# Performance work log

Measured on AMD Instinct MI355X. Metric: run time of the kernel, lower is better.

The kernel has to match this reference:

```python
import jax, jax.numpy as jnp
import numpy as np

N = 20000        # nodes
E = 320000       # edges (before self-loops)
V = 5000         # vocab size for each of the 5 categorical fields
L = 20           # padded token list length per node
SF = 16          # scalar feature count
ED = 32          # embedding_dim
HC = 128         # hidden_channels
NH = 4           # num_heads (conv1)
B = 8            # graphs in batch
DIN = SF + 5 * ED  # 176


def setup_inputs() -> dict:
    key = jax.random.key(0)
    ks = jax.random.split(key, 24)
    inp = {
        "x_scalar": jax.random.normal(ks[0], (N, SF), jnp.float32),
        "x_opcode": jax.random.randint(ks[1], (N, L), 0, V),
        "x_source": jax.random.randint(ks[2], (N, L), 0, V),
        "x_sink": jax.random.randint(ks[3], (N, L), 0, V),
        "x_string_manip": jax.random.randint(ks[4], (N, L), 0, V),
        "x_payload": jax.random.randint(ks[5], (N, L), 0, V),
        "edge_index": jax.random.randint(ks[6], (2, E), 0, N),
        "batch": jnp.sort(jax.random.randint(ks[7], (N,), 0, B)),
        # embedding tables (padding row 0 contributes nothing via the mask)
        "emb_opcode": jax.random.normal(ks[8], (V, ED), jnp.float32),
        "emb_source": jax.random.normal(ks[9], (V, ED), jnp.float32),
        "emb_sink": jax.random.normal(ks[10], (V, ED), jnp.float32),
        "emb_string_manip": jax.random.normal(ks[11], (V, ED), jnp.float32),
        "emb_payload": jax.random.normal(ks[12], (V, ED), jnp.float32),
        # LayerNorm params
        "ln_g": jnp.ones((DIN,), jnp.float32),
        "ln_b": jnp.zeros((DIN,), jnp.float32),
        # GATConv 1: in=DIN, out=HC, heads=NH
        "W1": jax.random.normal(ks[13], (DIN, NH * HC), jnp.float32) / np.sqrt(DIN),
        "a_src1": jax.random.normal(ks[14], (NH, HC), jnp.float32) / np.sqrt(HC),
        "a_dst1": jax.random.normal(ks[15], (NH, HC), jnp.float32) / np.sqrt(HC),
        "b1": jnp.zeros((NH * HC,), jnp.float32),
        # GATConv 2: in=NH*HC, out=HC, heads=1
        "W2": jax.random.normal(ks[16], (NH * HC, HC), jnp.float32) / np.sqrt(NH * HC),
        "a_src2": jax.random.normal(ks[17], (1, HC), jnp.float32) / np.sqrt(HC),
        "a_dst2": jax.random.normal(ks[18], (1, HC), jnp.float32) / np.sqrt(HC),
        "b2": jnp.zeros((HC,), jnp.float32),
    }
    return inp


def _masked_mean(table, idx):
    # embeds * (idx != 0) summed over token dim, divided by token count
    emb = table[idx]                                   # [N, L, ED]
    mask = (idx != 0).astype(table.dtype)[..., None]   # [N, L, 1]
    return (emb * mask).sum(1) / (mask.sum(1) + 1e-9)


def _layer_norm(x, g, b, eps=1e-5):
    mu = x.mean(-1, keepdims=True)
    var = ((x - mu) ** 2).mean(-1, keepdims=True)
    return (x - mu) * jax.lax.rsqrt(var + eps) * g + b


def _gat(x, src, dst, W, a_src, a_dst, bias, n):
    # PyG GATConv (eval mode: attention dropout off), self-loops already in src/dst
    h_, c = a_src.shape
    h = (x @ W).reshape(n, h_, c)                      # [N, H, C]
    al_s = (h * a_src).sum(-1)                         # [N, H]
    al_d = (h * a_dst).sum(-1)                         # [N, H]
    e = jax.nn.leaky_relu(al_s[src] + al_d[dst], 0.2)  # [E, H]
    m = jax.ops.segment_max(e, dst, num_segments=n)    # per-dst max for stability
    ex = jnp.exp(e - m[dst])
    den = jax.ops.segment_sum(ex, dst, num_segments=n)
    alpha = ex / (den[dst] + 1e-16)                    # per-dst softmax
    msg = h[src] * alpha[:, :, None]                   # [E, H, C]
    out = jax.ops.segment_sum(msg, dst, num_segments=n)
    return out.reshape(n, h_ * c) + bias


def reference(x_scalar, x_opcode, x_source, x_sink, x_string_manip, x_payload,
              edge_index, batch,
              emb_opcode, emb_source, emb_sink, emb_string_manip, emb_payload,
              ln_g, ln_b, W1, a_src1, a_dst1, b1, W2, a_src2, a_dst2, b2):
    n = x_scalar.shape[0]
    feats = jnp.concatenate([
        x_scalar,
        _masked_mean(emb_opcode, x_opcode),
        _masked_mean(emb_source, x_source),
        _masked_mean(emb_sink, x_sink),
        _masked_mean(emb_string_manip, x_string_manip),
        _masked_mean(emb_payload, x_payload),
    ], axis=1)                                         # [N, DIN]
    # GATConv adds self-loops by default
    loops = jnp.arange(n, dtype=edge_index.dtype)
    src = jnp.concatenate([edge_index[0], loops])
    dst = jnp.concatenate([edge_index[1], loops])
    x = jax.nn.elu(_gat(_layer_norm(feats, ln_g, ln_b), src, dst, W1, a_src1, a_dst1, b1, n))
    x = jax.nn.elu(_gat(x, src, dst, W2, a_src2, a_dst2, b2, n))
    return jax.ops.segment_max(x, batch, num_segments=B)  # global_max_pool -> [B, HC]
```

## Files before the change

### kernel.cpp

```cpp
#include <hip/hip_runtime.h>
#include <math.h>

#define SF 16
#define ED 32
#define LTOK 20
#define DIN 176
#define KP1 192
#define HC 128

typedef _Float16 f16x8 __attribute__((ext_vector_type(8)));
typedef _Float16 f16x2 __attribute__((ext_vector_type(2)));
typedef float f32x4 __attribute__((ext_vector_type(4)));

#if defined(__has_builtin)
#if __has_builtin(__builtin_amdgcn_fdot2)
#define HAVE_FDOT2 1
#endif
#endif

static __device__ __forceinline__ float leaky02(float x) { return x >= 0.f ? x : 0.2f * x; }
static __device__ __forceinline__ float eluf(float x)    { return x > 0.f ? x : expm1f(x); }
static __device__ __forceinline__ unsigned short f2h(float f)
{
  _Float16 h = (_Float16)f;
  return __builtin_bit_cast(unsigned short, h);
}
static __device__ __forceinline__ float h2f(unsigned short u)
{
  return (float)__builtin_bit_cast(_Float16, u);
}
static __device__ __forceinline__ float readlane_f(float v, int j)
{
  return __int_as_float(__builtin_amdgcn_readlane(__float_as_int(v), j));
}
static __device__ __forceinline__ unsigned readlane_u(unsigned v, int j)
{
  return (unsigned)__builtin_amdgcn_readlane((int)v, j);
}
#ifdef HAVE_FDOT2
static __device__ __forceinline__ float dot2(unsigned w, unsigned f, float c)
{
  return __builtin_amdgcn_fdot2(__builtin_bit_cast(f16x2, w),
                                __builtin_bit_cast(f16x2, f), c, false);
}
#endif

__global__ __launch_bounds__(256)
void prep_combined_kernel(const float* __restrict__ W1, const float* __restrict__ W2,
                          unsigned short* __restrict__ W1t, unsigned short* __restrict__ W2t,
                          const float* __restrict__ as1, const float* __restrict__ ad1,
                          float* __restrict__ vs, float* __restrict__ vd,
                          int* __restrict__ deg, unsigned* __restrict__ pool,
                          float* __restrict__ als2, float* __restrict__ ald2,
                          int N, int poolN)
{
  const int nb1 = (512 * KP1 + 255) / 256;
  const int nb2 = (HC * 512 + 255) / 256;
  const int nb3 = (N + 255) / 256;
  const int nb4 = (poolN + 255) / 256;
  int bid = blockIdx.x;
  if (bid < nb1) {
    int i = bid * 256 + threadIdx.x;
    if (i < 512 * KP1) {
      int n = i / KP1, k = i - n * KP1;
      W1t[i] = f2h((k < DIN) ? W1[(size_t)k * 512 + n] : 0.f);
    }
    return;
  }
  bid -= nb1;
  if (bid < nb2) {
    int i = bid * 256 + threadIdx.x;
    if (i < HC * 512) {
      int n = i / 512, k = i - n * 512;
      W2t[i] = f2h(W2[(size_t)k * HC + n]);
    }
    return;
  }
  bid -= nb2;
  if (bid < nb3) {
    int i = bid * 256 + threadIdx.x;
    if (i < N) { deg[i] = 0; als2[i] = 0.f; ald2[i] = 0.f; }
    return;
  }
  bid -= nb3;
  if (bid < nb4) {
    int i = bid * 256 + threadIdx.x;
    if (i < poolN) pool[i] = 0x00800000u;
    return;
  }
  bid -= nb4;
  {
    int k = bid;
    int h = threadIdx.x >> 6, lane = threadIdx.x & 63;
    const float* row = W1 + (size_t)k * 512 + h * HC;
    float s = row[lane] * as1[h * HC + lane] + row[lane + 64] * as1[h * HC + lane + 64];
    float d = row[lane] * ad1[h * HC + lane] + row[lane + 64] * ad1[h * HC + lane + 64];
    #pragma unroll
    for (int off = 32; off; off >>= 1) { s += __shfl_down(s, off); d += __shfl_down(d, off); }
    if (lane == 0) { vs[k * 4 + h] = s; vd[k * 4 + h] = d; }
  }
}

__global__ __launch_bounds__(256)
void feat_ln_kernel(const float* __restrict__ xs,
                    const int* __restrict__ i0, const int* __restrict__ i1,
                    const int* __restrict__ i2, const int* __restrict__ i3,
                    const int* __restrict__ i4,
                    const float* __restrict__ e0, const float* __restrict__ e1,
                    const float* __restrict__ e2, const float* __restrict__ e3,
                    const float* __restrict__ e4,
                    const float* __restrict__ g, const float* __restrict__ b,
                    const float4* __restrict__ vs, const float4* __restrict__ vd,
                    unsigned short* __restrict__ out,
                    float* __restrict__ als, float* __restrict__ ald, int N)
{
  __shared__ int toks[4][5 * LTOK];
  int w = threadIdx.x >> 6, l = threadIdx.x & 63;
  int n = blockIdx.x * 4 + w;
  if (n >= N) return;

  for (int q = l; q < 5 * LTOK; q += 64) {
    int f = q / LTOK, j = q - f * LTOK;
    const int* ip = (f == 0) ? i0 : (f == 1) ? i1 : (f == 2) ? i2 : (f == 3) ? i3 : i4;
    toks[w][q] = ip[n * LTOK + j];
  }

  float v[3];
  #pragma unroll
  for (int r = 0; r < 3; ++r) {
    int c = l + r * 64;
    float val = 0.f;
    if (c < SF) {
      val = xs[n * SF + c];
    } else if (c < DIN) {
      int f  = (c - SF) >> 5;
      int ch = (c - SF) & 31;
      const float* ep = (f == 0) ? e0 : (f == 1) ? e1 : (f == 2) ? e2 : (f == 3) ? e3 : e4;
      float vals[LTOK];
      #pragma unroll
      for (int j = 0; j < LTOK; ++j)
        vals[j] = ep[toks[w][f * LTOK + j] * ED + ch];
      float sum = 0.f, cnt = 0.f;
      #pragma unroll
      for (int j = 0; j < LTOK; ++j)
        if (toks[w][f * LTOK + j] != 0) { sum += vals[j]; cnt += 1.f; }
      val = sum / (cnt + 1e-9f);
    }
    v[r] = val;
  }

  float p  = v[0] + v[1] + v[2];
  float p2 = v[0] * v[0] + v[1] * v[1] + v[2] * v[2];
  #pragma unroll
  for (int off = 32; off; off >>= 1) { p += __shfl_xor(p, off); p2 += __shfl_xor(p2, off); }
  float mu   = p * (1.f / DIN);
  float var  = fmaxf(p2 * (1.f / DIN) - mu * mu, 0.f);
  float rstd = rsqrtf(var + 1e-5f);

  float pr[8] = {0.f, 0.f, 0.f, 0.f, 0.f, 0.f, 0.f, 0.f};
  #pragma unroll
  for (int r = 0; r < 3; ++r) {
    int c = l + r * 64;
    float y = 0.f;
    if (c < DIN) {
      y = (v[r] - mu) * rstd * g[c] + b[c];
      float4 s4 = vs[c], d4 = vd[c];
      pr[0] += y * s4.x; pr[1] += y * s4.y; pr[2] += y * s4.z; pr[3] += y * s4.w;
      pr[4] += y * d4.x; pr[5] += y * d4.y; pr[6] += y * d4.z; pr[7] += y * d4.w;
    }
    if (c < KP1) out[(size_t)n * KP1 + c] = f2h(y);
  }
  #pragma unroll
  for (int j = 0; j < 8; ++j)
    #pragma unroll
    for (int off = 32; off; off >>= 1) pr[j] += __shfl_xor(pr[j], off);
  if (l == 0) {
    als[n * 4 + 0] = pr[0]; als[n * 4 + 1] = pr[1];
    als[n * 4 + 2] = pr[2]; als[n * 4 + 3] = pr[3];
    ald[n * 4 + 0] = pr[4]; ald[n * 4 + 1] = pr[5];
    ald[n * 4 + 2] = pr[6]; ald[n * 4 + 3] = pr[7];
  }
}

__global__ void count_kernel(const int* __restrict__ ei, int E, int N, int* __restrict__ deg)
{
  int e = blockIdx.x * blockDim.x + threadIdx.x;
  if (e < E + N) {
    int dst = (e < E) ? ei[E + e] : (e - E);
    atomicAdd(&deg[dst], 1);
  }
}

__global__ __launch_bounds__(1024)
void scan_kernel(const int* __restrict__ deg, int* __restrict__ rowptr,
                 int* __restrict__ fill, int N)
{
  __shared__ int sums[1024];
  int t = threadIdx.x;
  int CH = (N + 1023) >> 10;
  int base = t * CH;
  int s = 0;
  for (int i = 0; i < CH; ++i) if (base + i < N) s += deg[base + i];
  sums[t] = s;
  __syncthreads();
  for (int off = 1; off < 1024; off <<= 1) {
    int v = (t >= off) ? sums[t - off] : 0;
    __syncthreads();
    sums[t] += v;
    __syncthreads();
  }
  int run = sums[t] - s;
  for (int i = 0; i < CH; ++i) {
    if (base + i < N) {
      rowptr[base + i] = run;
      fill[base + i]   = run;
      run += deg[base + i];
    }
  }
  if (t == 1023) rowptr[N] = run;
}

__global__ void scatter_kernel(const int* __restrict__ ei, int E, int N,
                               int* __restrict__ fill, int* __restrict__ csr_src)
{
  int e = blockIdx.x * blockDim.x + threadIdx.x;
  if (e < E + N) {
    int src, dst;
    if (e < E) { src = ei[e]; dst = ei[E + e]; }
    else       { src = dst = e - E; }
    int pos = atomicAdd(&fill[dst], 1);
    csr_src[pos] = src;
  }
}

__global__ __launch_bounds__(256)
void agg_feat_kernel(const unsigned short* __restrict__ F,
                     const float4* __restrict__ als, const float4* __restrict__ ald,
                     const int* __restrict__ rowptr, const int* __restrict__ csr_src,
                     unsigned short* __restrict__ G, int N)
{
  int wv = threadIdx.x >> 6, lane = threadIdx.x & 63;
  int n = blockIdx.x * 4 + wv;
  if (n >= N) return;
  int rs = __builtin_amdgcn_readfirstlane(rowptr[n]);
  int re = __builtin_amdgcn_readfirstlane(rowptr[n + 1]);
  int cnt = re - rs;
  float4 ad4 = ald[n];
  float aldv[4] = { ad4.x, ad4.y, ad4.z, ad4.w };

  float acc[4][4] = {};
  bool act = lane < 48;
  const unsigned short* Fb = F + lane * 4;

#ifdef HAVE_FDOT2
  auto passB = [&](int srcA, unsigned pkw[4], int ccnt) {
    for (int j = 0; j < ccnt; j += 4) {
      int s0 = __builtin_amdgcn_readlane(srcA, j);
      int s1 = __builtin_amdgcn_readlane(srcA, j + 1);
      int s2 = __builtin_amdgcn_readlane(srcA, j + 2);
      int s3 = __builtin_amdgcn_readlane(srcA, j + 3);
      unsigned wa0 = readlane_u(pkw[0], j), wb0 = readlane_u(pkw[0], j + 2);
      unsigned wa1 = readlane_u(pkw[1], j), wb1 = readlane_u(pkw[1], j + 2);
      unsigned wa2 = readlane_u(pkw[2], j), wb2 = readlane_u(pkw[2], j + 2);
      unsigned wa3 = readlane_u(pkw[3], j), wb3 = readlane_u(pkw[3], j + 2);
      if (act) {
        int2 a0 = *(const int2*)(Fb + (size_t)s0 * KP1);
        int2 a1 = *(const int2*)(Fb + (size_t)s1 * KP1);
        int2 a2 = *(const int2*)(Fb + (size_t)s2 * KP1);
        int2 a3 = *(const int2*)(Fb + (size_t)s3 * KP1);
        unsigned pA = __builtin_amdgcn_perm((unsigned)a0.x, (unsigned)a1.x, 0x01000504u);
        unsigned pB = __builtin_amdgcn_perm((unsigned)a0.x, (unsigned)a1.x, 0x03020706u);
        unsigned pC = __builtin_amdgcn_perm((unsigned)a0.y, (unsigned)a1.y, 0x01000504u);
        unsigned pD = __builtin_amdgcn_perm((unsigned)a0.y, (unsigned)a1.y, 0x03020706u);
        unsigned qA = __builtin_amdgcn_perm((unsigned)a2.x, (unsigned)a3.x, 0x01000504u);
        unsigned qB = __builtin_amdgcn_perm((unsigned)a2.x, (unsigned)a3.x, 0x03020706u);
        unsigned qC = __builtin_amdgcn_perm((unsigned)a2.y, (unsigned)a3.y, 0x01000504u);
        unsigned qD = __builtin_amdgcn_perm((unsigned)a2.y, (unsigned)a3.y, 0x03020706u);
        acc[0][0] = dot2(wa0, pA, acc[0][0]); acc[0][1] = dot2(wa0, pB, acc[0][1]);
        acc[0][2] = dot2(wa0, pC, acc[0][2]); acc[0][3] = dot2(wa0, pD, acc[0][3]);
        acc[1][0] = dot2(wa1, pA, acc[1][0]); acc[1][1] = dot2(wa1, pB, acc[1][1]);
        acc[1][2] = dot2(wa1, pC, acc[1][2]); acc[1][3] = dot2(wa1, pD, acc[1][3]);
        acc[2][0] = dot2(wa2, pA, acc[2][0]); acc[2][1] = dot2(wa2, pB, acc[2][1]);
        acc[2][2] = dot2(wa2, pC, acc[2][2]); acc[2][3] = dot2(wa2, pD, acc[2][3]);
        acc[3][0] = dot2(wa3, pA, acc[3][0]); acc[3][1] = dot2(wa3, pB, acc[3][1]);
        acc[3][2] = dot2(wa3, pC, acc[3][2]); acc[3][3] = dot2(wa3, pD, acc[3][3]);
        acc[0][0] = dot2(wb0, qA, acc[0][0]); acc[0][1] = dot2(wb0, qB, acc[0][1]);
        acc[0][2] = dot2(wb0, qC, acc[0][2]); acc[0][3] = dot2(wb0, qD, acc[0][3]);
        acc[1][0] = dot2(wb1, qA, acc[1][0]); acc[1][1] = dot2(wb1, qB, acc[1][1]);
        acc[1][2] = dot2(wb1, qC, acc[1][2]); acc[1][3] = dot2(wb1, qD, acc[1][3]);
        acc[2][0] = dot2(wb2, qA, acc[2][0]); acc[2][1] = dot2(wb2, qB, acc[2][1]);
        acc[2][2] = dot2(wb2, qC, acc[2][2]); acc[2][3] = dot2(wb2, qD, acc[2][3]);
        acc[3][0] = dot2(wb3, qA, acc[3][0]); acc[3][1] = dot2(wb3, qB, acc[3][1]);
        acc[3][2] = dot2(wb3, qC, acc[3][2]); acc[3][3] = dot2(wb3, qD, acc[3][3]);
      }
    }
  };
#else
  auto passB = [&](int srcA, float wf[4], int ccnt) {
    for (int j = 0; j < ccnt; ++j) {
      int src = __builtin_amdgcn_readlane(srcA, j);
      float q0 = readlane_f(wf[0], j), q1 = readlane_f(wf[1], j);
      float q2 = readlane_f(wf[2], j), q3 = readlane_f(wf[3], j);
      if (act) {
        int2 a0 = *(const int2*)(Fb + (size_t)src * KP1);
        float f0 = h2f((unsigned short)(a0.x & 0xffff));
        float f1 = h2f((unsigned short)((unsigned)a0.x >> 16));
        float f2v = h2f((unsigned short)(a0.y & 0xffff));
        float f3 = h2f((unsigned short)((unsigned)a0.y >> 16));
        acc[0][0] += q0 * f0; acc[0][1] += q0 * f1; acc[0][2] += q0 * f2v; acc[0][3] += q0 * f3;
        acc[1][0] += q1 * f0; acc[1][1] += q1 * f1; acc[1][2] += q1 * f2v; acc[1][3] += q1 * f3;
        acc[2][0] += q2 * f0; acc[2][1] += q2 * f1; acc[2][2] += q2 * f2v; acc[2][3] += q2 * f3;
        acc[3][0] += q3 * f0; acc[3][1] += q3 * f1; acc[3][2] += q3 * f2v; acc[3][3] += q3 * f3;
      }
    }
  };
#endif

  if (cnt <= 64) {
    int srcA = 0;
    float e[4] = { -1e30f, -1e30f, -1e30f, -1e30f };
    if (lane < cnt) {
      srcA = csr_src[rs + lane];
      float4 a4 = als[srcA];
      e[0] = leaky02(a4.x + aldv[0]); e[1] = leaky02(a4.y + aldv[1]);
      e[2] = leaky02(a4.z + aldv[2]); e[3] = leaky02(a4.w + aldv[3]);
    }
    float m[4] = { e[0], e[1], e[2], e[3] };
    #pragma unroll
    for (int off = 32; off; off >>= 1)
      #pragma unroll
      for (int h = 0; h < 4; ++h) m[h] = fmaxf(m[h], __shfl_xor(m[h], off));
    float w[4];
    #pragma unroll
    for (int h = 0; h < 4; ++h) w[h] = (lane < cnt) ? __expf(e[h] - m[h]) : 0.f;
    float den[4] = { w[0], w[1], w[2], w[3] };
    #pragma unroll
    for (int off = 32; off; off >>= 1)
      #pragma unroll
      for (int h = 0; h < 4; ++h) den[h] += __shfl_xor(den[h], off);
    #pragma unroll
    for (int h = 0; h < 4; ++h) w[h] /= (den[h] + 1e-16f);
#ifdef HAVE_FDOT2
    unsigned pkw[4];
    #pragma unroll
    for (int h = 0; h < 4; ++h) {
      float wn = __shfl_xor(w[h], 1);
      float we = (lane & 1) ? wn : w[h];
      float wo = (lane & 1) ? w[h] : wn;
      pkw[h] = (unsigned)f2h(we) | ((unsigned)f2h(wo) << 16);
    }
    passB(srcA, pkw, cnt);
#else
    passB(srcA, w, cnt);
#endif
  } else {
    float m[4], s[4];
    #pragma unroll
    for (int h = 0; h < 4; ++h) { m[h] = -1e30f; s[h] = 0.f; }
    for (int i = rs + lane; i < re; i += 64) {
      int src = csr_src[i];
      float4 a4 = als[src];
      float av[4] = { a4.x, a4.y, a4.z, a4.w };
      #pragma unroll
      for (int h = 0; h < 4; ++h) {
        float e = leaky02(av[h] + aldv[h]);
        float Mx = fmaxf(m[h], e);
        s[h] = s[h] * __expf(m[h] - Mx) + __expf(e - Mx);
        m[h] = Mx;
      }
    }
    #pragma unroll
    for (int off = 32; off; off >>= 1) {
      #pragma unroll
      for (int h = 0; h < 4; ++h) {
        float m2 = __shfl_xor(m[h], off);
        float s2 = __shfl_xor(s[h], off);
        float Mx = fmaxf(m[h], m2);
        s[h] = s[h] * __expf(m[h] - Mx) + s2 * __expf(m2 - Mx);
        m[h] = Mx;
      }
    }
    float inv[4];
    #pragma unroll
    for (int h = 0; h < 4; ++h) inv[h] = 1.f / (s[h] + 1e-16f);
    for (int b0 = rs; b0 < re; b0 += 64) {
      int bcnt = min(64, re - b0);
      int srcA = 0;
      float w[4] = {0.f, 0.f, 0.f, 0.f};
      if (lane < bcnt) {
        srcA = csr_src[b0 + lane];
        float4 a4 = als[srcA];
        w[0] = __expf(leaky02(a4.x + aldv[0]) - m[0]) * inv[0];
        w[1] = __expf(leaky02(a4.y + aldv[1]) - m[1]) * inv[1];
        w[2] = __expf(leaky02(a4.z + aldv[2]) - m[2]) * inv[2];
        w[3] = __expf(leaky02(a4.w + aldv[3]) - m[3]) * inv[3];
      }
#ifdef HAVE_FDOT2
      unsigned pkw[4];
      #pragma unroll
      for (int h = 0; h < 4; ++h) {
        float wn = __shfl_xor(w[h], 1);
        float we = (lane & 1) ? wn : w[h];
        float wo = (lane & 1) ? w[h] : wn;
        pkw[h] = (unsigned)f2h(we) | ((unsigned)f2h(wo) << 16);
      }
      passB(srcA, pkw, bcnt);
#else
      passB(srcA, w, bcnt);
#endif
    }
  }

  if (act) {
    #pragma unroll
    for (int h = 0; h < 4; ++h) {
      int2 o;
      o.x = (int)f2h(acc[h][0]) | ((int)f2h(acc[h][1]) << 16);
      o.y = (int)f2h(acc[h][2]) | ((int)f2h(acc[h][3]) << 16);
      *(int2*)&G[((size_t)h * N + n) * KP1 + lane * 4] = o;
    }
  }
}

template<int KPad, int BIAS_ELU, int LOGITS>
__global__ __launch_bounds__(256)
void gemm64_kernel(const unsigned short* __restrict__ A,
                   const unsigned short* __restrict__ Bt,
                   unsigned short* __restrict__ C,
                   int M, int Nc,
                   size_t aStrideZ, size_t bStrideZ, int cColStrideZ,
                   const float* __restrict__ bias,
                   const float* __restrict__ la_s, const float* __restrict__ la_d,
                   float* __restrict__ lout_s, float* __restrict__ lout_d)
{
  A  += blockIdx.z * aStrideZ;
  Bt += blockIdx.z * bStrideZ;
  const int colZ = blockIdx.z * cColStrideZ;

  __shared__ __align__(16) unsigned short As[2][4][520];
  __shared__ __align__(16) unsigned short Bs[2][4][520];

  const int tid  = threadIdx.x;
  const int lane = tid & 63, wv = tid >> 6;
  const int bm = blockIdx.y << 6, bn = blockIdx.x << 6;
  const int wm = (wv >> 1) << 5, wn = (wv & 1) << 5;
  const int kc = lane >> 4, r16 = lane & 15;

  const int srow = lane, skc = wv;
  const unsigned short* Ap = A + (size_t)(bm + srow) * KPad + skc * 8;
  const unsigned short* Bp = Bt + (size_t)(bn + srow) * KPad + skc * 8;
  const bool aok = (bm + srow) < M;

  f32x4 acc[2][2];
  #pragma unroll
  for (int m = 0; m < 2; ++m)
    #pragma unroll
    for (int n2 = 0; n2 < 2; ++n2) acc[m][n2] = (f32x4){0.f, 0.f, 0.f, 0.f};

  constexpr int NT = KPad / 32;
  int4 av = aok ? *(const int4*)Ap : make_int4(0, 0, 0, 0);
  int4 bv = *(const int4*)Bp;

  for (int t = 0; t < NT; ++t) {
    const int cur = t & 1;
    *(int4*)&As[cur][skc][srow * 8] = av;
    *(int4*)&Bs[cur][skc][srow * 8] = bv;
    if (t + 1 < NT) {
      av = aok ? *(const int4*)(Ap + (t + 1) * 32) : make_int4(0, 0, 0, 0);
      bv = *(const int4*)(Bp + (t + 1) * 32);
    }
    __syncthreads();
    f16x8 af0 = *(const f16x8*)&As[cur][kc][(wm + r16) * 8];
    f16x8 af1 = *(const f16x8*)&As[cur][kc][(wm + 16 + r16) * 8];
    f16x8 bf0 = *(const f16x8*)&Bs[cur][kc][(wn + r16) * 8];
    f16x8 bf1 = *(const f16x8*)&Bs[cur][kc][(wn + 16 + r16) * 8];
    acc[0][0] = __builtin_amdgcn_mfma_f32_16x16x32_f16(af0, bf0, acc[0][0], 0, 0, 0);
    acc[0][1] = __builtin_amdgcn_mfma_f32_16x16x32_f16(af0, bf1, acc[0][1], 0, 0, 0);
    acc[1][0] = __builtin_amdgcn_mfma_f32_16x16x32_f16(af1, bf0, acc[1][0], 0, 0, 0);
    acc[1][1] = __builtin_amdgcn_mfma_f32_16x16x32_f16(af1, bf1, acc[1][1], 0, 0, 0);
  }

  const int rq = lane >> 4;
  #pragma unroll
  for (int m = 0; m < 2; ++m) {
    #pragma unroll
    for (int r = 0; r < 4; ++r) {
      int row = bm + wm + m * 16 + rq * 4 + r;
      if (row < M) {
        #pragma unroll
        for (int n2 = 0; n2 < 2; ++n2) {
          int col = colZ + bn + wn + n2 * 16 + r16;
          float val = acc[m][n2][r];
          if (BIAS_ELU) { val += bias[col]; val = eluf(val); }
          C[(size_t)row * Nc + col] = f2h(val);
        }
      }
    }
  }

  if (LOGITS) {
    #pragma unroll
    for (int m = 0; m < 2; ++m) {
      #pragma unroll
      for (int r = 0; r < 4; ++r) {
        float ps = 0.f, pd = 0.f;
        #pragma unroll
        for (int n2 = 0; n2 < 2; ++n2) {
          int col = bn + wn + n2 * 16 + r16;
          float val = acc[m][n2][r];
          ps += val * la_s[col];
          pd += val * la_d[col];
        }
        #pragma unroll
        for (int off = 1; off < 16; off <<= 1) {
          ps += __shfl_xor(ps, off);
          pd += __shfl_xor(pd, off);
        }
        int row = bm + wm + m * 16 + rq * 4 + r;
        if (r16 == 0 && row < M) {
          atomicAdd(&lout_s[row], ps);
          atomicAdd(&lout_d[row], pd);
        }
      }
    }
  }
}

__global__ __launch_bounds__(256)
void agg_h2_kernel(const unsigned short* __restrict__ H,
                   const float* __restrict__ al_s, const float* __restrict__ al_d,
                   const int* __restrict__ rowptr, const int* __restrict__ csr_src,
                   const float* __restrict__ bias, unsigned short* __restrict__ out, int N)
{
  int wv = threadIdx.x >> 6, lane = threadIdx.x & 63;
  int n = blockIdx.x * 4 + wv;
  if (n >= N) return;
  int rs = __builtin_amdgcn_readfirstlane(rowptr[n]);
  int re = __builtin_amdgcn_readfirstlane(rowptr[n + 1]);
  int cnt = re - rs;
  float ald = al_d[n];
  float acc0 = 0.f, acc1 = 0.f;
  const unsigned short* Hb = H + lane * 2;

#ifdef HAVE_FDOT2
  auto passB = [&](int srcA, unsigned pkw, int ccnt) {
    for (int j = 0; j < ccnt; j += 4) {
      int s0 = __builtin_amdgcn_readlane(srcA, j);
      int s1 = __builtin_amdgcn_readlane(srcA, j + 1);
      int s2 = __builtin_amdgcn_readlane(srcA, j + 2);
      int s3 = __builtin_amdgcn_readlane(srcA, j + 3);
      unsigned pw0 = readlane_u(pkw, j);
      unsigned pw1 = readlane_u(pkw, j + 2);
      unsigned a0 = *(const unsigned*)(Hb + (size_t)s0 * HC);
      unsigned a1 = *(const unsigned*)(Hb + (size_t)s1 * HC);
      unsigned a2 = *(const unsigned*)(Hb + (size_t)s2 * HC);
      unsigned a3 = *(const unsigned*)(Hb + (size_t)s3 * HC);
      unsigned p0 = __builtin_amdgcn_perm(a0, a1, 0x01000504u);
      unsigned p1 = __builtin_amdgcn_perm(a0, a1, 0x03020706u);
      unsigned q0 = __builtin_amdgcn_perm(a2, a3, 0x01000504u);
      unsigned q1 = __builtin_amdgcn_perm(a2, a3, 0x03020706u);
      acc0 = dot2(pw0, p0, acc0);
      acc1 = dot2(pw0, p1, acc1);
      acc0 = dot2(pw1, q0, acc0);
      acc1 = dot2(pw1, q1, acc1);
    }
  };
#else
  auto passB = [&](int srcA, float wf, int ccnt) {
    for (int j = 0; j < ccnt; ++j) {
      int src = __builtin_amdgcn_readlane(srcA, j);
      float wgt = readlane_f(wf, j);
      unsigned a0 = *(const unsigned*)(Hb + (size_t)src * HC);
      acc0 += wgt * h2f((unsigned short)(a0 & 0xffff));
      acc1 += wgt * h2f((unsigned short)(a0 >> 16));
    }
  };
#endif

  if (cnt <= 64) {
    int srcA = 0;
    float e = -1e30f;
    if (lane < cnt) {
      srcA = csr_src[rs + lane];
      e = leaky02(al_s[srcA] + ald);
    }
    float m = e;
    #pragma unroll
    for (int off = 32; off; off >>= 1) m = fmaxf(m, __shfl_xor(m, off));
    float w = (lane < cnt) ? __expf(e - m) : 0.f;
    float den = w;
    #pragma unroll
    for (int off = 32; off; off >>= 1) den += __shfl_xor(den, off);
    w /= (den + 1e-16f);
#ifdef HAVE_FDOT2
    float wn2 = __shfl_xor(w, 1);
    float we = (lane & 1) ? wn2 : w;
    float wo = (lane & 1) ? w : wn2;
    unsigned pkw = (unsigned)f2h(we) | ((unsigned)f2h(wo) << 16);
    passB(srcA, pkw, cnt);
#else
    passB(srcA, w, cnt);
#endif
  } else {
    float m = -1e30f, s = 0.f;
    for (int i = rs + lane; i < re; i += 64) {
      int src = csr_src[i];
      float e = leaky02(al_s[src] + ald);
      float Mx = fmaxf(m, e);
      s = s * __expf(m - Mx) + __expf(e - Mx);
      m = Mx;
    }
    #pragma unroll
    for (int off = 32; off; off >>= 1) {
      float m2 = __shfl_xor(m, off);
      float s2 = __shfl_xor(s, off);
      float Mx = fmaxf(m, m2);
      s = s * __expf(m - Mx) + s2 * __expf(m2 - Mx);
      m = Mx;
    }
    float inv_den = 1.f / (s + 1e-16f);
    for (int c0 = rs; c0 < re; c0 += 64) {
      int ccnt = min(64, re - c0);
      int srcA = 0;
      float w = 0.f;
      if (lane < ccnt) {
        srcA = csr_src[c0 + lane];
        w = __expf(leaky02(al_s[srcA] + ald) - m) * inv_den;
      }
#ifdef HAVE_FDOT2
      float wn2 = __shfl_xor(w, 1);
      float we = (lane & 1) ? wn2 : w;
      float wo = (lane & 1) ? w : wn2;
      unsigned pkw = (unsigned)f2h(we) | ((unsigned)f2h(wo) << 16);
      passB(srcA, pkw, ccnt);
#else
      passB(srcA, w, ccnt);
#endif
    }
  }

  float o0 = eluf(acc0 + bias[lane * 2 + 0]);
  float o1 = eluf(acc1 + bias[lane * 2 + 1]);
  unsigned o = (unsigned)f2h(o0) | ((unsigned)f2h(o1) << 16);
  *(unsigned*)&out[(size_t)n * HC + lane * 2] = o;
}

static __device__ __forceinline__ unsigned enc_f(float f)
{
  unsigned u = __float_as_uint(f);
  return (u & 0x80000000u) ? ~u : (u | 0x80000000u);
}
static __device__ __forceinline__ float dec_f(unsigned u)
{
  return (u & 0x80000000u) ? __uint_as_float(u & 0x7fffffffu) : __uint_as_float(~u);
}

#define PNPB 128
__global__ __launch_bounds__(256)
void pool_seg_kernel(const unsigned short* __restrict__ x, const int* __restrict__ batch,
                     unsigned* __restrict__ pool, int N)
{
  int cp = (threadIdx.x & 63) * 2;
  int g  = threadIdx.x >> 6;
  int n0 = blockIdx.x * PNPB;
  int n1 = min(n0 + PNPB, N);
  int curb = -1;
  float m0 = 0.f, m1 = 0.f;
  for (int n = n0 + g; n < n1; n += 4) {
    int bg = batch[n];
    ushort2 v = *(const ushort2*)&x[(size_t)n * HC + cp];
    float v0 = h2f(v.x), v1 = h2f(v.y);
    if (bg != curb) {
      if (curb >= 0) {
        atomicMax(&pool[curb * HC + cp],     enc_f(m0));
        atomicMax(&pool[curb * HC + cp + 1], enc_f(m1));
      }
      curb = bg; m0 = v0; m1 = v1;
    } else {
      m0 = fmaxf(m0, v0);
      m1 = fmaxf(m1, v1);
    }
  }
  if (curb >= 0) {
    atomicMax(&pool[curb * HC + cp],     enc_f(m0));
    atomicMax(&pool[curb * HC + cp + 1], enc_f(m1));
  }
}

__global__ void pool_final_kernel(const unsigned* __restrict__ pool, float* __restrict__ out, int n)
{
  int i = blockIdx.x * blockDim.x + threadIdx.x;
  if (i < n) out[i] = dec_f(pool[i]);
}

extern "C" void kernel_launch(void* const* d_in, const int* in_sizes, int n_in,
                              void* d_out, int out_size, void* d_ws, size_t ws_size,
                              hipStream_t stream)
{
  const float* x_scalar = (const float*)d_in[0];
  const int* i0 = (const int*)d_in[1];
  const int* i1 = (const int*)d_in[2];
  const int* i2 = (const int*)d_in[3];
  const int* i3 = (const int*)d_in[4];
  const int* i4 = (const int*)d_in[5];
  const int* ei = (const int*)d_in[6];
  const int* batch = (const int*)d_in[7];
  const float* e0 = (const float*)d_in[8];
  const float* e1 = (const float*)d_in[9];
  const float* e2 = (const float*)d_in[10];
  const float* e3 = (const float*)d_in[11];
  const float* e4 = (const float*)d_in[12];
  const float* ln_g = (const float*)d_in[13];
  const float* ln_b = (const float*)d_in[14];
  const float* W1 = (const float*)d_in[15];
  const float* as1 = (const float*)d_in[16];
  const float* ad1 = (const float*)d_in[17];
  const float* b1 = (const float*)d_in[18];
  const float* W2 = (const float*)d_in[19];
  const float* as2 = (const float*)d_in[20];
  const float* ad2 = (const float*)d_in[21];
  const float* b2 = (const float*)d_in[22];

  const int N  = in_sizes[0] / SF;
  const int E  = in_sizes[6] / 2;
  const int Et = E + N;
  const int Bg = out_size / HC;
  const int MT64 = (N + 63) / 64;

  char* w = (char*)d_ws;
  auto alloc = [&](size_t bytes) -> char* {
    char* p = w;
    w += (bytes + 255) & ~(size_t)255;
    return p;
  };
  unsigned short* featsb = (unsigned short*)alloc((size_t)N * KP1 * 2);
  unsigned short* G      = (unsigned short*)alloc((size_t)4 * N * KP1 * 2);
  unsigned short* X2b    = (unsigned short*)alloc((size_t)N * 512 * 2);
  unsigned short* H2b    = (unsigned short*)alloc((size_t)N * HC * 2);
  unsigned short* X3b    = (unsigned short*)alloc((size_t)N * HC * 2);
  unsigned short* W1t    = (unsigned short*)alloc((size_t)512 * KP1 * 2);
  unsigned short* W2t    = (unsigned short*)alloc((size_t)HC * 512 * 2);
  float* vs      = (float*)alloc((size_t)KP1 * 4 * 4);
  float* vd      = (float*)alloc((size_t)KP1 * 4 * 4);
  float* als1    = (float*)alloc((size_t)N * 4 * 4);
  float* ald1    = (float*)alloc((size_t)N * 4 * 4);
  float* als2    = (float*)alloc((size_t)N * 4);
  float* ald2    = (float*)alloc((size_t)N * 4);
  int*   deg     = (int*)alloc((size_t)N * 4);
  int*   rowptr  = (int*)alloc((size_t)(N + 1) * 4);
  int*   fill    = (int*)alloc((size_t)N * 4);
  int*   csr_src = (int*)alloc((size_t)Et * 4);
  unsigned* pool = (unsigned*)alloc((size_t)Bg * HC * 4);

  {
    int nb1 = (512 * KP1 + 255) / 256;
    int nb2 = (HC * 512 + 255) / 256;
    int nb3 = (N + 255) / 256;
    int nb4 = (Bg * HC + 255) / 256;
    prep_combined_kernel<<<nb1 + nb2 + nb3 + nb4 + DIN, 256, 0, stream>>>(
        W1, W2, W1t, W2t, as1, ad1, vs, vd, deg, pool, als2, ald2, N, Bg * HC);
  }

  feat_ln_kernel<<<(N + 3) / 4, 256, 0, stream>>>(x_scalar, i0, i1, i2, i3, i4,
                                                  e0, e1, e2, e3, e4, ln_g, ln_b,
                                                  (const float4*)vs, (const float4*)vd,
                                                  featsb, als1, ald1, N);

  count_kernel<<<(Et + 255) / 256, 256, 0, stream>>>(ei, E, N, deg);
  scan_kernel<<<1, 1024, 0, stream>>>(deg, rowptr, fill, N);
  scatter_kernel<<<(Et + 255) / 256, 256, 0, stream>>>(ei, E, N, fill, csr_src);

  agg_feat_kernel<<<(N + 3) / 4, 256, 0, stream>>>(featsb, (const float4*)als1,
                                                   (const float4*)ald1,
                                                   rowptr, csr_src, G, N);
  gemm64_kernel<KP1, 1, 0><<<dim3(2, MT64, 4), 256, 0, stream>>>(
      G, W1t, X2b, N, 512, (size_t)N * KP1, (size_t)HC * KP1, HC, b1,
      nullptr, nullptr, nullptr, nullptr);

  gemm64_kernel<512, 0, 1><<<dim3(2, MT64, 1), 256, 0, stream>>>(
      X2b, W2t, H2b, N, HC, 0, 0, 0, nullptr,
      as2, ad2, als2, ald2);
  agg_h2_kernel<<<(N + 3) / 4, 256, 0, stream>>>(H2b, als2, ald2, rowptr, csr_src, b2, X3b, N);

  pool_seg_kernel<<<(N + PNPB - 1) / PNPB, 256, 0, stream>>>(X3b, batch, pool, N);
  pool_final_kernel<<<(Bg * HC + 255) / 256, 256, 0, stream>>>(pool, (float*)d_out, Bg * HC);
}
```

Before: 221.7 us.

## Fuse degree counting into feature/LayerNorm kernel and vectorize embedding gathers

Appends the edge-degree atomic counting blocks to the feat_ln kernel launch so that one launch does both jobs, and removes the separate count kernel. The embedding mean and LayerNorm path now has each lane handle two adjacent channels through float2 loads and packed half2 stores, which cuts the per-lane loop from 3 iterations to 2 and widens the memory accesses. This saves one launch and improves gather efficiency. In exchange, the heterogeneous blocks in one grid may contend for resources.

```diff
diff --git a/kernel.cpp b/kernel.cpp
--- a/kernel.cpp
+++ b/kernel.cpp
@@ -112,8 +112,19 @@
                     const float* __restrict__ g, const float* __restrict__ b,
                     const float4* __restrict__ vs, const float4* __restrict__ vd,
                     unsigned short* __restrict__ out,
-                    float* __restrict__ als, float* __restrict__ ald, int N)
-{
+                    float* __restrict__ als, float* __restrict__ ald,
+                    const int* __restrict__ ei, int E, int* __restrict__ deg,
+                    int nodeBlocks, int N)
+{
+  if (blockIdx.x >= nodeBlocks) {
+    int e = (blockIdx.x - nodeBlocks) * 256 + threadIdx.x;
+    if (e < E + N) {
+      int dst = (e < E) ? ei[E + e] : (e - E);
+      atomicAdd(&deg[dst], 1);
+    }
+    return;
+  }
+
   __shared__ int toks[4][5 * LTOK];
   int w = threadIdx.x >> 6, l = threadIdx.x & 63;
   int n = blockIdx.x * 4 + w;
@@ -125,50 +136,59 @@
     toks[w][q] = ip[n * LTOK + j];
   }
 
-  float v[3];
+  float2 v[2];
   #pragma unroll
-  for (int r = 0; r < 3; ++r) {
-    int c = l + r * 64;
-    float val = 0.f;
-    if (c < SF) {
-      val = xs[n * SF + c];
-    } else if (c < DIN) {
-      int f  = (c - SF) >> 5;
-      int ch = (c - SF) & 31;
+  for (int r = 0; r < 2; ++r) {
+    int p = l + r * 64;
+    float2 val = make_float2(0.f, 0.f);
+    if (p < 8) {
+      val = *(const float2*)&xs[n * SF + 2 * p];
+    } else if (p < 88) {
+      int c0 = 2 * p - 16;
+      int f  = c0 >> 5;
+      int ch = c0 & 31;
       const float* ep = (f == 0) ? e0 : (f == 1) ? e1 : (f == 2) ? e2 : (f == 3) ? e3 : e4;
-      float vals[LTOK];
+      float2 vals[LTOK];
       #pragma unroll
       for (int j = 0; j < LTOK; ++j)
-        vals[j] = ep[toks[w][f * LTOK + j] * ED + ch];
-      float sum = 0.f, cnt = 0.f;
+        vals[j] = *(const float2*)&ep[(size_t)toks[w][f * LTOK + j] * ED + ch];
+      float sx = 0.f, sy = 0.f, cntv = 0.f;
       #pragma unroll
       for (int j = 0; j < LTOK; ++j)
-        if (toks[w][f * LTOK + j] != 0) { sum += vals[j]; cnt += 1.f; }
-      val = sum / (cnt + 1e-9f);
+        if (toks[w][f * LTOK + j] != 0) { sx += vals[j].x; sy += vals[j].y; cntv += 1.f; }
+      float inv = 1.f / (cntv + 1e-9f);
+      val.x = sx * inv; val.y = sy * inv;
     }
     v[r] = val;
   }
 
-  float p  = v[0] + v[1] + v[2];
-  float p2 = v[0] * v[0] + v[1] * v[1] + v[2] * v[2];
+  float p1 = v[0].x + v[0].y + v[1].x + v[1].y;
+  float p2 = v[0].x * v[0].x + v[0].y * v[0].y + v[1].x * v[1].x + v[1].y * v[1].y;
   #pragma unroll
-  for (int off = 32; off; off >>= 1) { p += __shfl_xor(p, off); p2 += __shfl_xor(p2, off); }
-  float mu   = p * (1.f / DIN);
+  for (int off = 32; off; off >>= 1) { p1 += __shfl_xor(p1, off); p2 += __shfl_xor(p2, off); }
+  float mu   = p1 * (1.f / DIN);
   float var  = fmaxf(p2 * (1.f / DIN) - mu * mu, 0.f);
   float rstd = rsqrtf(var + 1e-5f);
 
   float pr[8] = {0.f, 0.f, 0.f, 0.f, 0.f, 0.f, 0.f, 0.f};
   #pragma unroll
-  for (int r = 0; r < 3; ++r) {
-    int c = l + r * 64;
-    float y = 0.f;
-    if (c < DIN) {
-      y = (v[r] - mu) * rstd * g[c] + b[c];
-      float4 s4 = vs[c], d4 = vd[c];
-      pr[0] += y * s4.x; pr[1] += y * s4.y; pr[2] += y * s4.z; pr[3] += y * s4.w;
-      pr[4] += y * d4.x; pr[5] += y * d4.y; pr[6] += y * d4.z; pr[7] += y * d4.w;
-    }
-    if (c < KP1) out[(size_t)n * KP1 + c] = f2h(y);
+  for (int r = 0; r < 2; ++r) {
+    int p = l + r * 64;
+    float y0 = 0.f, y1 = 0.f;
+    if (p < 88) {
+      int c = 2 * p;
+      y0 = (v[r].x - mu) * rstd * g[c] + b[c];
+      y1 = (v[r].y - mu) * rstd * g[c + 1] + b[c + 1];
+      float4 s0 = vs[c], s1 = vs[c + 1], d0 = vd[c], d1 = vd[c + 1];
+      pr[0] += y0 * s0.x + y1 * s1.x; pr[1] += y0 * s0.y + y1 * s1.y;
+      pr[2] += y0 * s0.z + y1 * s1.z; pr[3] += y0 * s0.w + y1 * s1.w;
+      pr[4] += y0 * d0.x + y1 * d1.x; pr[5] += y0 * d0.y + y1 * d1.y;
+      pr[6] += y0 * d0.z + y1 * d1.z; pr[7] += y0 * d0.w + y1 * d1.w;
+    }
+    if (p < 96) {
+      unsigned o = (unsigned)f2h(y0) | ((unsigned)f2h(y1) << 16);
+      *(unsigned*)&out[(size_t)n * KP1 + 2 * p] = o;
+    }
   }
   #pragma unroll
   for (int j = 0; j < 8; ++j)
@@ -179,15 +199,6 @@
     als[n * 4 + 2] = pr[2]; als[n * 4 + 3] = pr[3];
     ald[n * 4 + 0] = pr[4]; ald[n * 4 + 1] = pr[5];
     ald[n * 4 + 2] = pr[6]; ald[n * 4 + 3] = pr[7];
-  }
-}
-
-__global__ void count_kernel(const int* __restrict__ ei, int E, int N, int* __restrict__ deg)
-{
-  int e = blockIdx.x * blockDim.x + threadIdx.x;
-  if (e < E + N) {
-    int dst = (e < E) ? ei[E + e] : (e - E);
-    atomicAdd(&deg[dst], 1);
   }
 }
 
@@ -761,12 +772,15 @@
         W1, W2, W1t, W2t, as1, ad1, vs, vd, deg, pool, als2, ald2, N, Bg * HC);
   }
 
-  feat_ln_kernel<<<(N + 3) / 4, 256, 0, stream>>>(x_scalar, i0, i1, i2, i3, i4,
-                                                  e0, e1, e2, e3, e4, ln_g, ln_b,
-                                                  (const float4*)vs, (const float4*)vd,
-                                                  featsb, als1, ald1, N);
-
-  count_kernel<<<(Et + 255) / 256, 256, 0, stream>>>(ei, E, N, deg);
+  {
+    int nodeBlocks  = (N + 3) / 4;
+    int countBlocks = (Et + 255) / 256;
+    feat_ln_kernel<<<nodeBlocks + countBlocks, 256, 0, stream>>>(
+        x_scalar, i0, i1, i2, i3, i4, e0, e1, e2, e3, e4, ln_g, ln_b,
+        (const float4*)vs, (const float4*)vd, featsb, als1, ald1,
+        ei, E, deg, nodeBlocks, N);
+  }
+
   scan_kernel<<<1, 1024, 0, stream>>>(deg, rowptr, fill, N);
   scatter_kernel<<<(Et + 255) / 256, 256, 0, stream>>>(ei, E, N, fill, csr_src);
 
```

Result: no change. 220.0 us (-0.8%).
